# Kernel tuning notes

Measured on AMD Instinct MI355X. Metric: run time of the kernel, lower is better.

Reference implementation:

```python
import jax, jax.numpy as jnp
import numpy as np
import math

B, S, CIN, H, W = 8, 8, 64, 32, 32
COUT, K = 128, 3
PW = COUT * CIN * K * K  # 73728
P = PW + COUT            # 73856


def setup_inputs() -> dict:
    key = jax.random.key(0)
    ks = jax.random.split(key, 6)
    return {
        "x": jax.random.normal(ks[0], (B, S, CIN, H, W), dtype=jnp.float32),
        "e": jax.random.normal(ks[1], (S, P), dtype=jnp.float32),
        "mu_w": jax.random.normal(ks[2], (PW,), dtype=jnp.float32) * 0.02,
        "rho_w": jax.random.normal(ks[3], (PW,), dtype=jnp.float32) * 0.5,
        "mu_b": jax.random.normal(ks[4], (COUT,), dtype=jnp.float32) * 0.02,
        "rho_b": jax.random.normal(ks[5], (COUT,), dtype=jnp.float32) * 0.5,
    }


def _unit_log_mfg(v):
    # v: [s_n, D]; -log(2*pi)*D/2 - sum(v**2)/2  (scalar, matching torch code)
    two_pi = jnp.asarray(2.0 * math.pi, v.dtype)
    return -jnp.log(two_pi) * (v.shape[1] / 2.0) - jnp.sum(v * v) / 2.0


def reference(x, e, mu_w, rho_w, mu_b, rho_b):
    s_n = e.shape[0]
    cout = mu_b.shape[0]
    cin = x.shape[2]
    k = int(round(math.sqrt(mu_w.shape[0] / (cout * cin))))
    pw = mu_w.shape[0]

    sig_w = jax.nn.softplus(rho_w)  # log(1+exp(rho))
    sig_b = jax.nn.softplus(rho_b)
    w = mu_w[None, :] + sig_w[None, :] * e[:, :pw]          # [s_n, PW]
    b = mu_b[None, :] + sig_b[None, :] * e[:, pw:pw + cout]  # [s_n, COUT]

    entropy_q = jnp.sum(jnp.log(sig_w)) + jnp.sum(jnp.log(sig_b))
    cross_entropy_qp = _unit_log_mfg(w) + _unit_log_mfg(b)
    kl_qp = -entropy_q - cross_entropy_qp

    w5 = w.reshape(s_n, cout, cin, k, k)  # per-sample OIHW kernels

    # per-sample conv: vmap over the sample axis j; batch conv over data axis i
    def conv_one(xj, wj):  # xj [B,CIN,H,W], wj [COUT,CIN,K,K]
        return jax.lax.conv(xj, wj, (1, 1), 'VALID')

    out = jax.vmap(conv_one, in_axes=(1, 0), out_axes=1)(x, w5)  # [B,S,COUT,H',W']
    out = out + b[None, :, :, None, None]
    return out, kl_qp
```

## Files before the change

### kernel.cpp

```cpp
#include <hip/hip_runtime.h>
#include <hip/hip_bf16.h>
#include <math.h>

#define Bn    8
#define Sn    8
#define COUTc 128
#define PWc   73728
#define Pc    73856
#define WOc   30
#define NPIX  900
#define GPIX  7200
#define NSTEP 9
#define TILE  64
#define NTIL  113

typedef __bf16 bf16;
typedef bf16  bf16x8 __attribute__((ext_vector_type(8)));
typedef float f32x16 __attribute__((ext_vector_type(16)));

__device__ __forceinline__ float softplus_f(float x) {
    return fmaxf(x, 0.f) + log1pf(expf(-fabsf(x)));
}

__device__ __forceinline__ unsigned int pack2(float a, float b) {
    unsigned short ua = __builtin_bit_cast(unsigned short, (bf16)a);
    unsigned short ub = __builtin_bit_cast(unsigned short, (bf16)b);
    return ((unsigned int)ub << 16) | (unsigned int)ua;
}

__device__ __forceinline__ void gl16(const void* g, void* l) {
    typedef __attribute__((address_space(1))) void gvoid;
    typedef __attribute__((address_space(3))) void lvoid;
    __builtin_amdgcn_global_load_lds((gvoid*)g, (lvoid*)l, 16, 0, 0);
}

__global__ __launch_bounds__(256) void prep_all(
        const float* __restrict__ xg, const float* __restrict__ e,
        const float* __restrict__ mu_w, const float* __restrict__ rho_w,
        const float* __restrict__ mu_b, const float* __restrict__ rho_b,
        bf16* __restrict__ xt, bf16* __restrict__ wimg,
        float* __restrict__ bq, float* __restrict__ slots) {
    const int bid = blockIdx.x;
    const int t   = threadIdx.x;

    if (bid < 512) {
        const int img  = bid >> 3;
        const int part = bid & 7;
        const int p    = part * 128 + (t >> 1);
        const int half = t & 1;
        const float* src = xg + ((size_t)img << 16) + (size_t)(half * 32) * 1024 + p;
        bf16*        dst = xt + ((size_t)img << 16) + (size_t)p * 64 + half * 32;
        #pragma unroll
        for (int o = 0; o < 4; ++o) {
            uint4 pk;
            pk.x = pack2(src[(o * 8 + 0) * 1024], src[(o * 8 + 1) * 1024]);
            pk.y = pack2(src[(o * 8 + 2) * 1024], src[(o * 8 + 3) * 1024]);
            pk.z = pack2(src[(o * 8 + 4) * 1024], src[(o * 8 + 5) * 1024]);
            pk.w = pack2(src[(o * 8 + 6) * 1024], src[(o * 8 + 7) * 1024]);
            *reinterpret_cast<uint4*>(dst + o * 8) = pk;
        }
        return;
    }

    float ls = 0.f, sq = 0.f;
    if (bid < 544) {
        const int gidx = (bid - 512) * 256 + t;
        const int co   = gidx >> 6;
        const int ci   = gidx & 63;
        const int p0   = co * 576 + ci * 9;
        float mu[9], sg[9];
        #pragma unroll
        for (int r = 0; r < 9; ++r) {
            mu[r] = mu_w[p0 + r];
            sg[r] = softplus_f(rho_w[p0 + r]);
            ls   += logf(sg[r]);
        }
        const int dstp = (co << 6) + (((ci >> 3) ^ (co & 7)) << 3) + (ci & 7);
        #pragma unroll
        for (int s = 0; s < Sn; ++s) {
            const float* es = e + s * Pc + p0;
            #pragma unroll
            for (int r = 0; r < 9; ++r) {
                float wv = fmaf(sg[r], es[r], mu[r]);
                wimg[((s * NSTEP + r) << 13) + dstp] = (bf16)wv;
                sq += wv * wv;
            }
        }
    } else {
        if (t < COUTc) {
            float sig = softplus_f(rho_b[t]);
            ls = logf(sig);
            float mu = mu_b[t];
            #pragma unroll
            for (int s = 0; s < Sn; ++s) {
                float bv = fmaf(sig, e[s * Pc + PWc + t], mu);
                bq[s * COUTc + t] = bv;
                sq += bv * bv;
            }
        }
    }

    #pragma unroll
    for (int off = 32; off > 0; off >>= 1) {
        ls += __shfl_down(ls, off);
        sq += __shfl_down(sq, off);
    }
    __shared__ float sls[4], ssq[4];
    const int lane = t & 63, wd = t >> 6;
    if (lane == 0) { sls[wd] = ls; ssq[wd] = sq; }
    __syncthreads();
    if (t == 0) {
        slots[2 * (bid - 512)]     = sls[0] + sls[1] + sls[2] + sls[3];
        slots[2 * (bid - 512) + 1] = ssq[0] + ssq[1] + ssq[2] + ssq[3];
    }
}

__global__ __launch_bounds__(256) void conv_mfma(
        const bf16* __restrict__ xt, const bf16* __restrict__ wimg,
        const float* __restrict__ bq, const float* __restrict__ slots,
        float* __restrict__ out, float* __restrict__ klout) {
    const int bid  = blockIdx.x;
    const int s    = bid & 7;
    const int tile = bid >> 3;
    const int t    = threadIdx.x;
    const int lane = t & 63;
    const int w    = t >> 6;
    const int wr   = w >> 1;
    const int wc   = w & 1;

    __shared__ bf16 Wbuf[2][8192];
    __shared__ bf16 Xbuf[2][4096];

    const char* wsrcL = (const char*)wimg + ((size_t)(s * NSTEP) << 14)
                      + (w << 12) + (lane << 4);

    const char *x0, *x1;
    #pragma unroll
    for (int q = 0; q < 2; ++q) {
        int pix = w * 16 + q * 8 + (lane >> 3);
        int g   = tile * TILE + pix;
        if (g >= GPIX) g = GPIX - 1;
        int b2 = g / NPIX, rr = g - b2 * NPIX, oy = rr / WOc, ox = rr - oy * WOc;
        int m  = (lane & 7) ^ (pix & 7);
        const char* ptr = (const char*)xt
            + ((((size_t)(b2 * Sn + s) << 10) + oy * 32 + ox) << 7) + (m << 4);
        if (q == 0) x0 = ptr; else x1 = ptr;
    }

    f32x16 acc[2];
    #pragma unroll
    for (int i = 0; i < 2; ++i)
        #pragma unroll
        for (int k = 0; k < 16; ++k)
            acc[i][k] = 0.f;

    #define STAGE(stepc, b)                                                  \
    {                                                                        \
        const char* ws_ = wsrcL + ((stepc) << 14);                           \
        char* wl_ = (char*)(&Wbuf[(b)][0]) + (w << 12);                      \
        gl16(ws_,        wl_);                                               \
        gl16(ws_ + 1024, wl_ + 1024);                                        \
        gl16(ws_ + 2048, wl_ + 2048);                                        \
        gl16(ws_ + 3072, wl_ + 3072);                                        \
        const int roff_ = (((stepc) / 3) * 32 + ((stepc) % 3)) * 128;        \
        char* xl_ = (char*)(&Xbuf[(b)][0]) + (w << 11);                      \
        gl16(x0 + roff_, xl_);                                               \
        gl16(x1 + roff_, xl_ + 1024);                                        \
    }

    #define COMPUTE(b)                                                       \
    {                                                                        \
        const bf16* Wl_ = &Wbuf[(b)][0];                                     \
        const bf16* Xl_ = &Xbuf[(b)][0];                                     \
        _Pragma("unroll")                                                    \
        for (int kc = 0; kc < 4; ++kc) {                                     \
            const int oct_ = ((kc << 1) + (lane >> 5)) ^ (lane & 7);         \
            bf16x8 af0 = *reinterpret_cast<const bf16x8*>(                   \
                Wl_ + ((wr * 64 + (lane & 31)) << 6) + (oct_ << 3));         \
            bf16x8 af1 = *reinterpret_cast<const bf16x8*>(                   \
                Wl_ + ((wr * 64 + 32 + (lane & 31)) << 6) + (oct_ << 3));    \
            bf16x8 bf0 = *reinterpret_cast<const bf16x8*>(                   \
                Xl_ + ((wc * 32 + (lane & 31)) << 6) + (oct_ << 3));         \
            acc[0] = __builtin_amdgcn_mfma_f32_32x32x16_bf16(af0, bf0, acc[0], 0, 0, 0); \
            acc[1] = __builtin_amdgcn_mfma_f32_32x32x16_bf16(af1, bf0, acc[1], 0, 0, 0); \
        }                                                                    \
    }

    STAGE(0, 0);
    STAGE(1, 1);

    #define ITER(tt, b)                                                      \
        asm volatile("s_waitcnt vmcnt(6)" ::: "memory");                     \
        __builtin_amdgcn_s_barrier();                                        \
        __builtin_amdgcn_sched_barrier(0);                                   \
        COMPUTE(b);                                                          \
        __builtin_amdgcn_sched_barrier(0);                                   \
        __builtin_amdgcn_s_barrier();                                        \
        STAGE((tt) + 2, b);

    ITER(0, 0)
    ITER(1, 1)
    ITER(2, 0)
    ITER(3, 1)
    ITER(4, 0)
    ITER(5, 1)
    ITER(6, 0)
    asm volatile("s_waitcnt vmcnt(6)" ::: "memory");
    __builtin_amdgcn_s_barrier();
    __builtin_amdgcn_sched_barrier(0);
    COMPUTE(1);
    asm volatile("s_waitcnt vmcnt(0)" ::: "memory");
    __builtin_amdgcn_s_barrier();
    __builtin_amdgcn_sched_barrier(0);
    COMPUTE(0);

    #undef ITER
    #undef COMPUTE
    #undef STAGE

    const int colp = lane & 31;
    const int hi   = lane >> 5;
    const int gg   = tile * TILE + wc * 32 + colp;
    if (gg < GPIX) {
        const int b2 = gg / NPIX;
        const int r2 = gg - b2 * NPIX;
        float* ob = out + (size_t)(b2 * Sn + s) * (COUTc * NPIX) + r2;
        #pragma unroll
        for (int ti = 0; ti < 2; ++ti) {
            #pragma unroll
            for (int reg = 0; reg < 16; ++reg) {
                int co = wr * 64 + ti * 32 + (reg & 3) + 8 * (reg >> 2) + 4 * hi;
                ob[co * NPIX] = acc[ti][reg] + bq[s * COUTc + co];
            }
        }
    }

    if (bid == 0 && t == 0) {
        float ls = 0.f, sq = 0.f;
        for (int i2 = 0; i2 < 33; ++i2) {
            ls += slots[2 * i2];
            sq += slots[2 * i2 + 1];
        }
        *klout = -ls + 0.91893853320467274f * (float)Pc + 0.5f * sq;
    }
}

extern "C" void kernel_launch(void* const* d_in, const int* in_sizes, int n_in,
                              void* d_out, int out_size, void* d_ws, size_t ws_size,
                              hipStream_t stream) {
    const float* x     = (const float*)d_in[0];
    const float* e     = (const float*)d_in[1];
    const float* mu_w  = (const float*)d_in[2];
    const float* rho_w = (const float*)d_in[3];
    const float* mu_b  = (const float*)d_in[4];
    const float* rho_b = (const float*)d_in[5];
    float* out = (float*)d_out;

    bf16*  wimg  = (bf16*)d_ws;
    float* bq    = (float*)((char*)d_ws + 1179648);
    float* slots = (float*)((char*)d_ws + 1183744);
    bf16*  xt    = (bf16*)((char*)d_ws + 1187840);

    prep_all<<<dim3(545), dim3(256), 0, stream>>>(
        x, e, mu_w, rho_w, mu_b, rho_b, xt, wimg, bq, slots);

    conv_mfma<<<dim3(NTIL * Sn), dim3(256), 0, stream>>>(
        xt, wimg, bq, slots, out, out + (out_size - 1));
}
```

Baseline: 35.93 us.

## Stage input row window in LDS once and double pixel tile to 128

The conv kernel now loads a window of ten input rows per image once into LDS (channel-octet planes) and reads every 3x3 tap from that window, instead of re-gathering shifted pixel tiles for each of the 9 steps. The pixel tile grows from 64 to 128, so each wave computes a 2x2 grid of MFMA tiles and the grid shrinks to 57 tiles per sample. The prep kernel switches to vectorized float4 reads and writes x in a channel-octet-planar bf16 layout to match. The cost is more LDS per block and fewer blocks, which may lower occupancy, plus extra logic for tiles that cross an image boundary.

```diff
diff --git a/kernel.cpp b/kernel.cpp
--- a/kernel.cpp
+++ b/kernel.cpp
@@ -11,11 +11,15 @@
 #define NPIX  900
 #define GPIX  7200
 #define NSTEP 9
-#define TILE  64
-#define NTIL  113
+#define TILE  128
+#define NT2   57
+#define WSLOTS 10
+#define XPLANE (WSLOTS * 32 * 16)
+#define XLDSB  (8 * XPLANE)
 
 typedef __bf16 bf16;
 typedef bf16  bf16x8 __attribute__((ext_vector_type(8)));
+typedef float f32x4v __attribute__((ext_vector_type(4)));
 typedef float f32x16 __attribute__((ext_vector_type(16)));
 
 __device__ __forceinline__ float softplus_f(float x) {
@@ -46,18 +50,26 @@
     if (bid < 512) {
         const int img  = bid >> 3;
         const int part = bid & 7;
-        const int p    = part * 128 + (t >> 1);
-        const int half = t & 1;
-        const float* src = xg + ((size_t)img << 16) + (size_t)(half * 32) * 1024 + p;
-        bf16*        dst = xt + ((size_t)img << 16) + (size_t)p * 64 + half * 32;
-        #pragma unroll
-        for (int o = 0; o < 4; ++o) {
+        const int oct  = t >> 5;
+        const int p0   = part * 128 + (t & 31) * 4;
+        const float* src = xg + ((size_t)img << 16) + (size_t)(oct * 8) * 1024 + p0;
+        f32x4v v0 = *reinterpret_cast<const f32x4v*>(src);
+        f32x4v v1 = *reinterpret_cast<const f32x4v*>(src + 1024);
+        f32x4v v2 = *reinterpret_cast<const f32x4v*>(src + 2048);
+        f32x4v v3 = *reinterpret_cast<const f32x4v*>(src + 3072);
+        f32x4v v4 = *reinterpret_cast<const f32x4v*>(src + 4096);
+        f32x4v v5 = *reinterpret_cast<const f32x4v*>(src + 5120);
+        f32x4v v6 = *reinterpret_cast<const f32x4v*>(src + 6144);
+        f32x4v v7 = *reinterpret_cast<const f32x4v*>(src + 7168);
+        char* dst = (char*)xt + (size_t)img * 131072 + oct * 16384 + p0 * 16;
+        #pragma unroll
+        for (int i = 0; i < 4; ++i) {
             uint4 pk;
-            pk.x = pack2(src[(o * 8 + 0) * 1024], src[(o * 8 + 1) * 1024]);
-            pk.y = pack2(src[(o * 8 + 2) * 1024], src[(o * 8 + 3) * 1024]);
-            pk.z = pack2(src[(o * 8 + 4) * 1024], src[(o * 8 + 5) * 1024]);
-            pk.w = pack2(src[(o * 8 + 6) * 1024], src[(o * 8 + 7) * 1024]);
-            *reinterpret_cast<uint4*>(dst + o * 8) = pk;
+            pk.x = pack2(v0[i], v1[i]);
+            pk.y = pack2(v2[i], v3[i]);
+            pk.z = pack2(v4[i], v5[i]);
+            pk.w = pack2(v6[i], v7[i]);
+            *reinterpret_cast<uint4*>(dst + i * 16) = pk;
         }
         return;
     }
@@ -127,34 +139,23 @@
     const int w    = t >> 6;
     const int wr   = w >> 1;
     const int wc   = w & 1;
+    const int hi   = lane >> 5;
+    const int lo   = lane & 31;
 
     __shared__ bf16 Wbuf[2][8192];
-    __shared__ bf16 Xbuf[2][4096];
+    __shared__ char Xw[XLDSB];
+
+    const int g0 = tile * TILE;
+    const int R0 = g0 / 30;
+    const int bA = R0 / 30;
+    const int rA = R0 - bA * 30;
+    const int nA = 30 - rA;
+    const bool crossing = (rA >= 25);
 
     const char* wsrcL = (const char*)wimg + ((size_t)(s * NSTEP) << 14)
                       + (w << 12) + (lane << 4);
 
-    const char *x0, *x1;
-    #pragma unroll
-    for (int q = 0; q < 2; ++q) {
-        int pix = w * 16 + q * 8 + (lane >> 3);
-        int g   = tile * TILE + pix;
-        if (g >= GPIX) g = GPIX - 1;
-        int b2 = g / NPIX, rr = g - b2 * NPIX, oy = rr / WOc, ox = rr - oy * WOc;
-        int m  = (lane & 7) ^ (pix & 7);
-        const char* ptr = (const char*)xt
-            + ((((size_t)(b2 * Sn + s) << 10) + oy * 32 + ox) << 7) + (m << 4);
-        if (q == 0) x0 = ptr; else x1 = ptr;
-    }
-
-    f32x16 acc[2];
-    #pragma unroll
-    for (int i = 0; i < 2; ++i)
-        #pragma unroll
-        for (int k = 0; k < 16; ++k)
-            acc[i][k] = 0.f;
-
-    #define STAGE(stepc, b)                                                  \
+    #define STAGEW(stepc, b)                                                 \
     {                                                                        \
         const char* ws_ = wsrcL + ((stepc) << 14);                           \
         char* wl_ = (char*)(&Wbuf[(b)][0]) + (w << 12);                      \
@@ -162,41 +163,74 @@
         gl16(ws_ + 1024, wl_ + 1024);                                        \
         gl16(ws_ + 2048, wl_ + 2048);                                        \
         gl16(ws_ + 3072, wl_ + 3072);                                        \
-        const int roff_ = (((stepc) / 3) * 32 + ((stepc) % 3)) * 128;        \
-        char* xl_ = (char*)(&Xbuf[(b)][0]) + (w << 11);                      \
-        gl16(x0 + roff_, xl_);                                               \
-        gl16(x1 + roff_, xl_ + 1024);                                        \
-    }
-
-    #define COMPUTE(b)                                                       \
+    }
+
+    {
+        const char* xtB = (const char*)xt;
+        #pragma unroll
+        for (int r = 0; r < 5; ++r) {
+            int slot = 2 * r + hi;
+            int b, iy;
+            if (crossing && slot >= nA + 2) { b = bA + 1; iy = slot - nA - 2; }
+            else { b = bA; iy = rA + slot; if (iy > 31) iy = 31; }
+            if (b > 7) b = 7;
+            const char* src = xtB + (size_t)(b * 8 + s) * 131072
+                            + (size_t)(w * 2) * 16384 + (iy * 32 + lo) * 16;
+            gl16(src,         Xw + (w * 2) * XPLANE + r * 1024);
+            gl16(src + 16384, Xw + (w * 2 + 1) * XPLANE + r * 1024);
+        }
+    }
+
+    STAGEW(0, 0);
+    STAGEW(1, 1);
+
+    int xb0, xb1;
+    #pragma unroll
+    for (int j = 0; j < 2; ++j) {
+        int g = g0 + wc * 64 + j * 32 + lo;
+        if (g > GPIX - 1) g = GPIX - 1;
+        int R = g / 30, col = g - R * 30;
+        int b = R / 30, oy = R - b * 30;
+        int slot0 = (b == bA) ? (oy - rA) : (nA + 2 + oy);
+        int base = hi * XPLANE + (slot0 * 32 + col) * 16;
+        if (j == 0) xb0 = base; else xb1 = base;
+    }
+
+    f32x16 acc00, acc01, acc10, acc11;
+    #pragma unroll
+    for (int k = 0; k < 16; ++k) {
+        acc00[k] = 0.f; acc01[k] = 0.f; acc10[k] = 0.f; acc11[k] = 0.f;
+    }
+
+    #define COMPUTE(b, KY, KX)                                               \
     {                                                                        \
         const bf16* Wl_ = &Wbuf[(b)][0];                                     \
-        const bf16* Xl_ = &Xbuf[(b)][0];                                     \
         _Pragma("unroll")                                                    \
         for (int kc = 0; kc < 4; ++kc) {                                     \
-            const int oct_ = ((kc << 1) + (lane >> 5)) ^ (lane & 7);         \
+            const int oct_ = ((kc << 1) + hi) ^ (lane & 7);                  \
             bf16x8 af0 = *reinterpret_cast<const bf16x8*>(                   \
-                Wl_ + ((wr * 64 + (lane & 31)) << 6) + (oct_ << 3));         \
+                Wl_ + ((wr * 64 + lo) << 6) + (oct_ << 3));                  \
             bf16x8 af1 = *reinterpret_cast<const bf16x8*>(                   \
-                Wl_ + ((wr * 64 + 32 + (lane & 31)) << 6) + (oct_ << 3));    \
+                Wl_ + ((wr * 64 + 32 + lo) << 6) + (oct_ << 3));             \
             bf16x8 bf0 = *reinterpret_cast<const bf16x8*>(                   \
-                Xl_ + ((wc * 32 + (lane & 31)) << 6) + (oct_ << 3));         \
-            acc[0] = __builtin_amdgcn_mfma_f32_32x32x16_bf16(af0, bf0, acc[0], 0, 0, 0); \
-            acc[1] = __builtin_amdgcn_mfma_f32_32x32x16_bf16(af1, bf0, acc[1], 0, 0, 0); \
+                Xw + xb0 + kc * (2 * XPLANE) + ((KY) * 512 + (KX) * 16));    \
+            bf16x8 bf1 = *reinterpret_cast<const bf16x8*>(                   \
+                Xw + xb1 + kc * (2 * XPLANE) + ((KY) * 512 + (KX) * 16));    \
+            acc00 = __builtin_amdgcn_mfma_f32_32x32x16_bf16(af0, bf0, acc00, 0, 0, 0); \
+            acc01 = __builtin_amdgcn_mfma_f32_32x32x16_bf16(af0, bf1, acc01, 0, 0, 0); \
+            acc10 = __builtin_amdgcn_mfma_f32_32x32x16_bf16(af1, bf0, acc10, 0, 0, 0); \
+            acc11 = __builtin_amdgcn_mfma_f32_32x32x16_bf16(af1, bf1, acc11, 0, 0, 0); \
         }                                                                    \
     }
 
-    STAGE(0, 0);
-    STAGE(1, 1);
-
     #define ITER(tt, b)                                                      \
-        asm volatile("s_waitcnt vmcnt(6)" ::: "memory");                     \
+        asm volatile("s_waitcnt vmcnt(4)" ::: "memory");                     \
         __builtin_amdgcn_s_barrier();                                        \
         __builtin_amdgcn_sched_barrier(0);                                   \
-        COMPUTE(b);                                                          \
+        COMPUTE(b, (tt) / 3, (tt) % 3);                                      \
         __builtin_amdgcn_sched_barrier(0);                                   \
         __builtin_amdgcn_s_barrier();                                        \
-        STAGE((tt) + 2, b);
+        STAGEW((tt) + 2, b);
 
     ITER(0, 0)
     ITER(1, 1)
@@ -205,32 +239,39 @@
     ITER(4, 0)
     ITER(5, 1)
     ITER(6, 0)
-    asm volatile("s_waitcnt vmcnt(6)" ::: "memory");
+    asm volatile("s_waitcnt vmcnt(4)" ::: "memory");
     __builtin_amdgcn_s_barrier();
     __builtin_amdgcn_sched_barrier(0);
-    COMPUTE(1);
+    COMPUTE(1, 2, 1);
     asm volatile("s_waitcnt vmcnt(0)" ::: "memory");
     __builtin_amdgcn_s_barrier();
     __builtin_amdgcn_sched_barrier(0);
-    COMPUTE(0);
+    COMPUTE(0, 2, 2);
 
     #undef ITER
     #undef COMPUTE
-    #undef STAGE
-
-    const int colp = lane & 31;
-    const int hi   = lane >> 5;
-    const int gg   = tile * TILE + wc * 32 + colp;
-    if (gg < GPIX) {
-        const int b2 = gg / NPIX;
-        const int r2 = gg - b2 * NPIX;
-        float* ob = out + (size_t)(b2 * Sn + s) * (COUTc * NPIX) + r2;
-        #pragma unroll
-        for (int ti = 0; ti < 2; ++ti) {
+    #undef STAGEW
+
+    #pragma unroll
+    for (int ti = 0; ti < 2; ++ti) {
+        float bs[16];
+        #pragma unroll
+        for (int reg = 0; reg < 16; ++reg) {
+            int co = wr * 64 + ti * 32 + (reg & 3) + 8 * (reg >> 2) + 4 * hi;
+            bs[reg] = bq[s * COUTc + co];
+        }
+        #pragma unroll
+        for (int tj = 0; tj < 2; ++tj) {
+            const f32x16& av = ti ? (tj ? acc11 : acc10) : (tj ? acc01 : acc00);
+            int gg = tile * TILE + wc * 64 + tj * 32 + lo;
+            if (gg >= GPIX) continue;
+            int b2 = gg / NPIX;
+            int r2 = gg - b2 * NPIX;
+            float* ob = out + (size_t)(b2 * Sn + s) * (COUTc * NPIX) + r2;
             #pragma unroll
             for (int reg = 0; reg < 16; ++reg) {
                 int co = wr * 64 + ti * 32 + (reg & 3) + 8 * (reg >> 2) + 4 * hi;
-                ob[co * NPIX] = acc[ti][reg] + bq[s * COUTc + co];
+                ob[co * NPIX] = av[reg] + bs[reg];
             }
         }
     }
@@ -264,6 +305,6 @@
     prep_all<<<dim3(545), dim3(256), 0, stream>>>(
         x, e, mu_w, rho_w, mu_b, rho_b, xt, wimg, bq, slots);
 
-    conv_mfma<<<dim3(NTIL * Sn), dim3(256), 0, stream>>>(
+    conv_mfma<<<dim3(NT2 * Sn), dim3(256), 0, stream>>>(
         xt, wimg, bq, slots, out, out + (out_size - 1));
 }
```

Measured after the change: 34.72 us. 1.03x faster.
